# Performance work log

Hardware: AMD Instinct MI355X
Metric: run time of the kernel (lower is better)

## Reference

```python
import jax, jax.numpy as jnp
import numpy as np

D_MODEL = 1024
NUM_HEADS = 16
H_DIM = 4096
EPS = 1e-5


def setup_inputs() -> dict:
    key = jax.random.key(0)
    ks = jax.random.split(key, 16)
    B, S, D, H = 2, 2048, D_MODEL, H_DIM
    s = 0.02
    return {
        "x": jax.random.normal(ks[0], (B, S, D), jnp.float32),
        "wq": jax.random.normal(ks[1], (D, D), jnp.float32) * s,
        "bq": jnp.zeros((D,), jnp.float32),
        "wk": jax.random.normal(ks[2], (D, D), jnp.float32) * s,
        "bk": jnp.zeros((D,), jnp.float32),
        "wv": jax.random.normal(ks[3], (D, D), jnp.float32) * s,
        "bv": jnp.zeros((D,), jnp.float32),
        "wo": jax.random.normal(ks[4], (D, D), jnp.float32) * s,
        "bo": jnp.zeros((D,), jnp.float32),
        "ln1_g": jnp.ones((D,), jnp.float32),
        "ln1_b": jnp.zeros((D,), jnp.float32),
        "w1": jax.random.normal(ks[5], (H, D), jnp.float32) * s,
        "b1": jnp.zeros((H,), jnp.float32),
        "w2": jax.random.normal(ks[6], (D, H), jnp.float32) * s,
        "b2": jnp.zeros((D,), jnp.float32),
        "ln2_g": jnp.ones((D,), jnp.float32),
        "ln2_b": jnp.zeros((D,), jnp.float32),
    }


def _layer_norm(x, g, b):
    mu = jnp.mean(x, axis=-1, keepdims=True)
    var = jnp.mean(jnp.square(x - mu), axis=-1, keepdims=True)
    return (x - mu) * jax.lax.rsqrt(var + EPS) * g + b


def _mhsa(x, wq, bq, wk, bk, wv, bv, wo, bo):
    B, S, D = x.shape
    Hh, hd = NUM_HEADS, D // NUM_HEADS
    q = (x @ wq.T + bq).reshape(B, S, Hh, hd)
    k = (x @ wk.T + bk).reshape(B, S, Hh, hd)
    v = (x @ wv.T + bv).reshape(B, S, Hh, hd)
    scale = hd ** -0.5
    scores = jnp.einsum('bqhd,bkhd->bhqk', q, k) * scale
    att = jax.nn.softmax(scores, axis=-1)
    out = jnp.einsum('bhqk,bkhd->bqhd', att, v).reshape(B, S, D)
    return out @ wo.T + bo


def reference(x, wq, bq, wk, bk, wv, bv, wo, bo, ln1_g, ln1_b,
              w1, b1, w2, b2, ln2_g, ln2_b):
    # pre-norm variant as written in the torch source:
    # x = norm1(x); x = x + msa(x)  (residual uses NORMALIZED x)
    x = _layer_norm(x, ln1_g, ln1_b)
    x = x + _mhsa(x, wq, bq, wk, bk, wv, bv, wo, bo)
    x = _layer_norm(x, ln2_g, ln2_b)
    h = jax.nn.gelu(x @ w1.T + b1, approximate=False)
    x = x + (h @ w2.T + b2)
    return x
```

## Files before the change

### kernel.cpp

```cpp
#include <hip/hip_runtime.h>
#include <hip/hip_bf16.h>

typedef unsigned short u16;
typedef __attribute__((ext_vector_type(8))) short short8;
typedef __attribute__((ext_vector_type(4))) float f32x4;

#define DM 1024
#define HM 4096
#define NHEADS 16
#define HD 64
#define SQ 2048
#define NBATCH 2
#define NTOK 4096

#define NX  ((size_t)NTOK * DM)

__device__ __forceinline__ u16 f2b(float f) {
    union { float f; unsigned int i; } w; w.f = f;
    unsigned int x = w.i;
    return (u16)((x + 0x7FFFu + ((x >> 16) & 1u)) >> 16);
}
__device__ __forceinline__ u16 f2b_ru(float f) {
    union { float f; unsigned int i; } w; w.f = f;
    return (u16)((w.i + 0x8000u) >> 16);
}

__device__ __forceinline__ void gload_lds16(const void* g, void* l) {
    __builtin_amdgcn_global_load_lds(
        (const __attribute__((address_space(1))) void*)g,
        (__attribute__((address_space(3))) void*)l, 16, 0, 0);
}

__global__ void cvt_all(const float* __restrict__ wq, const float* __restrict__ wk,
                        const float* __restrict__ wv, const float* __restrict__ wo,
                        const float* __restrict__ w1, const float* __restrict__ w2,
                        const float* __restrict__ bq, const float* __restrict__ bk,
                        const float* __restrict__ bv, float* __restrict__ bias_dst,
                        u16* __restrict__ dst) {
    const int NW4 = DM * DM / 4;
    int i = blockIdx.x * 256 + threadIdx.x;
    if (i < 12 * NW4) {
        const float* src; int base; float sc = 1.0f;
        if      (i <     NW4) { src = wq; base = 0;       sc = 0.125f; }
        else if (i < 2 * NW4) { src = wk; base = NW4; }
        else if (i < 3 * NW4) { src = wv; base = 2 * NW4; }
        else if (i < 4 * NW4) { src = wo; base = 3 * NW4; }
        else if (i < 8 * NW4) { src = w1; base = 4 * NW4; }
        else                  { src = w2; base = 8 * NW4; }
        float4 f = ((const float4*)src)[i - base];
        ushort4 o;
        o.x = f2b(f.x * sc); o.y = f2b(f.y * sc);
        o.z = f2b(f.z * sc); o.w = f2b(f.w * sc);
        ((ushort4*)dst)[i] = o;
    } else {
        int j = i - 12 * NW4;
        if (j < 3 * DM) {
            float v = (j < DM) ? bq[j] * 0.125f
                    : (j < 2 * DM) ? bk[j - DM] : bv[j - 2 * DM];
            bias_dst[j] = v;
        }
    }
}

__global__ void ln_kernel(const float* __restrict__ xin, const float* __restrict__ g,
                          const float* __restrict__ b, float* __restrict__ outf,
                          u16* __restrict__ outb) {
    int t = blockIdx.x, tid = threadIdx.x;
    float4 f = ((const float4*)(xin + (size_t)t * DM))[tid];
    float v0 = f.x, v1 = f.y, v2 = f.z, v3 = f.w;
    float s  = v0 + v1 + v2 + v3;
    float ss = v0*v0 + v1*v1 + v2*v2 + v3*v3;
    #pragma unroll
    for (int o = 32; o > 0; o >>= 1) {
        s  += __shfl_down(s,  o, 64);
        ss += __shfl_down(ss, o, 64);
    }
    __shared__ float rs[4], rss[4];
    int w = tid >> 6, lane = tid & 63;
    if (!lane) { rs[w] = s; rss[w] = ss; }
    __syncthreads();
    s  = rs[0] + rs[1] + rs[2] + rs[3];
    ss = rss[0] + rss[1] + rss[2] + rss[3];
    float mean = s * (1.0f / DM);
    float var  = ss * (1.0f / DM) - mean * mean;
    float rstd = rsqrtf(var + 1e-5f);
    float4 gu = ((const float4*)g)[tid];
    float4 bu = ((const float4*)b)[tid];
    float4 o;
    o.x = (v0 - mean) * rstd * gu.x + bu.x;
    o.y = (v1 - mean) * rstd * gu.y + bu.y;
    o.z = (v2 - mean) * rstd * gu.z + bu.z;
    o.w = (v3 - mean) * rstd * gu.w + bu.w;
    ((float4*)(outf + (size_t)t * DM))[tid] = o;
    ushort4 ob; ob.x = f2b(o.x); ob.y = f2b(o.y); ob.z = f2b(o.z); ob.w = f2b(o.w);
    ((ushort4*)(outb + (size_t)t * DM))[tid] = ob;
}

__global__ void vtr_kernel(const u16* __restrict__ qkv, u16* __restrict__ vT) {
    __shared__ u16 tile[64][72];
    int bid = blockIdx.x;
    int tt = bid & 31, bh = bid >> 5;
    int h = bh & (NHEADS - 1), b = bh >> 4;
    int tid = threadIdx.x;
    int r = tid >> 2, c0 = (tid & 3) << 4;
    const u16* src = qkv + ((size_t)(b * SQ + tt * 64 + r)) * (3 * DM) + 2 * DM + h * HD + c0;
    #pragma unroll
    for (int j = 0; j < 4; j++)
        *(ushort4*)&tile[r][c0 + (j << 2)] = *(const ushort4*)(src + (j << 2));
    __syncthreads();
    int dd = tid >> 2, t0 = (tid & 3) << 4;
    u16* dst = vT + ((size_t)bh * HD + dd) * SQ + tt * 64 + t0;
    #pragma unroll
    for (int j = 0; j < 4; j++) {
        ushort4 v;
        v.x = tile[t0 + (j << 2) + 0][dd];
        v.y = tile[t0 + (j << 2) + 1][dd];
        v.z = tile[t0 + (j << 2) + 2][dd];
        v.w = tile[t0 + (j << 2) + 3][dd];
        *(ushort4*)(dst + (j << 2)) = v;
    }
}

template<int GELU, int RESID, int OUTBF>
__global__ __launch_bounds__(256, 3)
void gemm_bt(const u16* __restrict__ A, const u16* __restrict__ W,
             const float* __restrict__ bias, const float* __restrict__ resid,
             void* __restrict__ Cout, int M, int N, int K) {
    __shared__ __attribute__((aligned(16))) u16 As[128 * 64];
    __shared__ __attribute__((aligned(16))) u16 Bs[128 * 64];
    int tid  = threadIdx.x;
    int wid  = tid >> 6, lane = tid & 63;
    int m0 = blockIdx.y << 7, n0 = blockIdx.x << 7;
    int wm = (wid & 1) << 6, wn = (wid >> 1) << 6;

    int rIn = lane >> 3;
    int cIn = (lane & 7) << 3;
    int s0  = wid << 2;
    int fr = lane & 15;
    int fc = (lane >> 4) << 3;

    f32x4 acc[4][4];
    #pragma unroll
    for (int i = 0; i < 4; i++)
        #pragma unroll
        for (int j = 0; j < 4; j++)
            acc[i][j] = (f32x4){0.f, 0.f, 0.f, 0.f};

    for (int k0 = 0; k0 < K; k0 += 64) {
        #pragma unroll
        for (int t = 0; t < 4; t++) {
            int s = s0 + t;
            gload_lds16(A + (size_t)(m0 + (s << 3) + rIn) * K + k0 + cIn, As + (s << 9));
            gload_lds16(W + (size_t)(n0 + (s << 3) + rIn) * K + k0 + cIn, Bs + (s << 9));
        }
        __syncthreads();
        #pragma unroll
        for (int ch = 0; ch < 2; ch++) {
            int kc = (ch << 5) + fc;
            short8 af[4], bf[4];
            #pragma unroll
            for (int mi = 0; mi < 4; mi++)
                af[mi] = *(const short8*)(As + (size_t)(wm + (mi << 4) + fr) * 64 + kc);
            #pragma unroll
            for (int ni = 0; ni < 4; ni++)
                bf[ni] = *(const short8*)(Bs + (size_t)(wn + (ni << 4) + fr) * 64 + kc);
            #pragma unroll
            for (int mi = 0; mi < 4; mi++)
                #pragma unroll
                for (int ni = 0; ni < 4; ni++)
                    acc[mi][ni] = __builtin_amdgcn_mfma_f32_16x16x32_bf16(
                        af[mi], bf[ni], acc[mi][ni], 0, 0, 0);
        }
        __syncthreads();
    }

    int erow = (lane >> 4) << 2;
    #pragma unroll
    for (int ni = 0; ni < 4; ni++) {
        int col = n0 + wn + (ni << 4) + fr;
        float bv = bias[col];
        #pragma unroll
        for (int mi = 0; mi < 4; mi++) {
            #pragma unroll
            for (int r = 0; r < 4; r++) {
                int row = m0 + wm + (mi << 4) + erow + r;
                float val = acc[mi][ni][r] + bv;
                if (GELU)  val = 0.5f * val * (1.0f + erff(val * 0.70710678118654752f));
                if (RESID) val += resid[(size_t)row * N + col];
                if (OUTBF) ((u16*)Cout)[(size_t)row * N + col] = f2b(val);
                else       ((float*)Cout)[(size_t)row * N + col] = val;
            }
        }
    }
}

template<int GELU, int RESID, int OUTBF>
__global__ __launch_bounds__(256, 3)
void gemm_n64(const u16* __restrict__ A, const u16* __restrict__ W,
              const float* __restrict__ bias, const float* __restrict__ resid,
              void* __restrict__ Cout, int M, int N, int K) {
    __shared__ __attribute__((aligned(16))) u16 As[128 * 64];
    __shared__ __attribute__((aligned(16))) u16 Bs[64 * 64];
    int tid  = threadIdx.x;
    int wid  = tid >> 6, lane = tid & 63;
    int m0 = blockIdx.y << 7, n0 = blockIdx.x << 6;
    int wm = (wid & 1) << 6, wn = (wid >> 1) << 5;

    int rIn = lane >> 3;
    int cIn = (lane & 7) << 3;
    int sA = wid << 2;
    int sB = wid << 1;
    int fr = lane & 15;
    int fc = (lane >> 4) << 3;

    f32x4 acc[4][2];
    #pragma unroll
    for (int i = 0; i < 4; i++)
        #pragma unroll
        for (int j = 0; j < 2; j++)
            acc[i][j] = (f32x4){0.f, 0.f, 0.f, 0.f};

    for (int k0 = 0; k0 < K; k0 += 64) {
        #pragma unroll
        for (int t = 0; t < 4; t++) {
            int s = sA + t;
            gload_lds16(A + (size_t)(m0 + (s << 3) + rIn) * K + k0 + cIn, As + (s << 9));
        }
        #pragma unroll
        for (int t = 0; t < 2; t++) {
            int s = sB + t;
            gload_lds16(W + (size_t)(n0 + (s << 3) + rIn) * K + k0 + cIn, Bs + (s << 9));
        }
        __syncthreads();
        #pragma unroll
        for (int ch = 0; ch < 2; ch++) {
            int kc = (ch << 5) + fc;
            short8 af[4], bf[2];
            #pragma unroll
            for (int mi = 0; mi < 4; mi++)
                af[mi] = *(const short8*)(As + (size_t)(wm + (mi << 4) + fr) * 64 + kc);
            #pragma unroll
            for (int ni = 0; ni < 2; ni++)
                bf[ni] = *(const short8*)(Bs + (size_t)(wn + (ni << 4) + fr) * 64 + kc);
            #pragma unroll
            for (int mi = 0; mi < 4; mi++)
                #pragma unroll
                for (int ni = 0; ni < 2; ni++)
                    acc[mi][ni] = __builtin_amdgcn_mfma_f32_16x16x32_bf16(
                        af[mi], bf[ni], acc[mi][ni], 0, 0, 0);
        }
        __syncthreads();
    }

    int erow = (lane >> 4) << 2;
    #pragma unroll
    for (int ni = 0; ni < 2; ni++) {
        int col = n0 + wn + (ni << 4) + fr;
        float bv = bias[col];
        #pragma unroll
        for (int mi = 0; mi < 4; mi++) {
            #pragma unroll
            for (int r = 0; r < 4; r++) {
                int row = m0 + wm + (mi << 4) + erow + r;
                float val = acc[mi][ni][r] + bv;
                if (GELU)  val = 0.5f * val * (1.0f + erff(val * 0.70710678118654752f));
                if (RESID) val += resid[(size_t)row * N + col];
                if (OUTBF) ((u16*)Cout)[(size_t)row * N + col] = f2b(val);
                else       ((float*)Cout)[(size_t)row * N + col] = val;
            }
        }
    }
}

__global__ __launch_bounds__(256) void fattn_mfma(const u16* __restrict__ QKV,
                                                  const u16* __restrict__ VT,
                                                  u16* __restrict__ O) {
    __shared__ __attribute__((aligned(16))) u16 QP[4096];
    __shared__ __attribute__((aligned(16))) u16 Ks[2][4096];
    __shared__ __attribute__((aligned(16))) u16 Vt[2][4096];
    const int ld = 3 * DM;
    int bid = blockIdx.x;
    int qt = bid & 31, bh = bid >> 5;
    int h = bh & (NHEADS - 1), b = bh >> 4;
    int tid = threadIdx.x, wid = tid >> 6, lane = tid & 63;
    int fr = lane & 15;
    int fcs = (((lane >> 4) ^ ((fr >> 1) & 3)) << 3);
    int lsw = (((lane & 3) ^ ((lane >> 3) & 3)) << 3);
    size_t tokb = (size_t)b * SQ;
    const u16* Qg  = QKV + tokb * ld + h * HD;
    const u16* Kg  = QKV + tokb * ld + DM + h * HD;
    const u16* VTg = VT + ((size_t)bh * HD) * SQ;
    int s0 = wid << 1;
    u16* Ps = QP + (wid << 10);

    {
        #pragma unroll
        for (int t = 0; t < 2; t++) {
            int s = s0 + t;
            const u16* g = Qg + (size_t)(qt * 64 + ((s & 3) << 4) + (lane >> 2)) * ld
                         + ((s >> 2) << 5) + lsw;
            gload_lds16(g, QP + (s << 9));
        }
    }
    {
        #pragma unroll
        for (int t = 0; t < 2; t++) {
            int s = s0 + t;
            const u16* g = Kg + (size_t)(((s & 3) << 4) + (lane >> 2)) * ld
                         + ((s >> 2) << 5) + lsw;
            gload_lds16(g, Ks[0] + (s << 9));
            const u16* gv = VTg + (size_t)(((s & 3) << 4) + (lane >> 2)) * SQ
                          + ((s >> 2) << 5) + lsw;
            gload_lds16(gv, Vt[0] + (s << 9));
        }
    }
    f32x4 oacc[4];
    #pragma unroll
    for (int di = 0; di < 4; di++) oacc[di] = (f32x4){0.f, 0.f, 0.f, 0.f};
    float lsum[4] = {0.f, 0.f, 0.f, 0.f};
    __syncthreads();
    short8 aq0 = *(const short8*)(QP + ((wid << 4) + fr) * 32 + fcs);
    short8 aq1 = *(const short8*)(QP + 2048 + ((wid << 4) + fr) * 32 + fcs);
    __syncthreads();

    for (int kt = 0; kt < SQ / 64; kt++) {
        int buf = kt & 1;
        if (kt + 1 < SQ / 64) {
            #pragma unroll
            for (int t = 0; t < 2; t++) {
                int s = s0 + t;
                const u16* g = Kg + (size_t)((kt + 1) * 64 + ((s & 3) << 4) + (lane >> 2)) * ld
                             + ((s >> 2) << 5) + lsw;
                gload_lds16(g, Ks[buf ^ 1] + (s << 9));
                const u16* gv = VTg + (size_t)(((s & 3) << 4) + (lane >> 2)) * SQ
                              + (kt + 1) * 64 + ((s >> 2) << 5) + lsw;
                gload_lds16(gv, Vt[buf ^ 1] + (s << 9));
            }
        }
        #pragma unroll
        for (int ni = 0; ni < 4; ni++) {
            short8 bk0 = *(const short8*)(Ks[buf] + ((ni << 4) + fr) * 32 + fcs);
            short8 bk1 = *(const short8*)(Ks[buf] + 2048 + ((ni << 4) + fr) * 32 + fcs);
            f32x4 z = (f32x4){0.f, 0.f, 0.f, 0.f};
            __builtin_amdgcn_s_setprio(1);
            z = __builtin_amdgcn_mfma_f32_16x16x32_bf16(aq0, bk0, z, 0, 0, 0);
            z = __builtin_amdgcn_mfma_f32_16x16x32_bf16(aq1, bk1, z, 0, 0, 0);
            __builtin_amdgcn_s_setprio(0);
            int c  = (ni << 4) + fr;
            int cb = (c >> 5) << 9;
            int khi = (c & 31) >> 3, klo = c & 7;
            #pragma unroll
            for (int r = 0; r < 4; r++) {
                float e = __expf(z[r]);
                lsum[r] += e;
                int row = ((lane >> 4) << 2) + r;
                Ps[cb + row * 32 + ((khi ^ ((row >> 1) & 3)) << 3) + klo] = f2b_ru(e);
            }
        }
        short8 ap0 = *(const short8*)(Ps + fr * 32 + fcs);
        short8 ap1 = *(const short8*)(Ps + 512 + fr * 32 + fcs);
        __builtin_amdgcn_s_setprio(1);
        #pragma unroll
        for (int di = 0; di < 4; di++) {
            short8 bv0 = *(const short8*)(Vt[buf] + ((di << 4) + fr) * 32 + fcs);
            short8 bv1 = *(const short8*)(Vt[buf] + 2048 + ((di << 4) + fr) * 32 + fcs);
            oacc[di] = __builtin_amdgcn_mfma_f32_16x16x32_bf16(ap0, bv0, oacc[di], 0, 0, 0);
            oacc[di] = __builtin_amdgcn_mfma_f32_16x16x32_bf16(ap1, bv1, oacc[di], 0, 0, 0);
        }
        __builtin_amdgcn_s_setprio(0);
        __syncthreads();
    }
    #pragma unroll
    for (int msk = 1; msk <= 8; msk <<= 1)
        #pragma unroll
        for (int r = 0; r < 4; r++) lsum[r] += __shfl_xor(lsum[r], msk, 64);
    float inv[4];
    #pragma unroll
    for (int r = 0; r < 4; r++) inv[r] = 1.0f / lsum[r];
    #pragma unroll
    for (int di = 0; di < 4; di++) {
        int d = (di << 4) + fr;
        #pragma unroll
        for (int r = 0; r < 4; r++) {
            int q = qt * 64 + (wid << 4) + ((lane >> 4) << 2) + r;
            O[(tokb + q) * DM + h * HD + d] = f2b(oacc[di][r] * inv[r]);
        }
    }
}

extern "C" void kernel_launch(void* const* d_in, const int* in_sizes, int n_in,
                              void* d_out, int out_size, void* d_ws, size_t ws_size,
                              hipStream_t stream) {
    if (n_in < 17) return;
    const float* x   = (const float*)d_in[0];
    const float* wq  = (const float*)d_in[1];
    const float* bq  = (const float*)d_in[2];
    const float* wk  = (const float*)d_in[3];
    const float* bk  = (const float*)d_in[4];
    const float* wv  = (const float*)d_in[5];
    const float* bv  = (const float*)d_in[6];
    const float* wo  = (const float*)d_in[7];
    const float* bo  = (const float*)d_in[8];
    const float* g1  = (const float*)d_in[9];
    const float* e1  = (const float*)d_in[10];
    const float* w1  = (const float*)d_in[11];
    const float* b1  = (const float*)d_in[12];
    const float* w2  = (const float*)d_in[13];
    const float* b2  = (const float*)d_in[14];
    const float* g2  = (const float*)d_in[15];
    const float* e2  = (const float*)d_in[16];

    float* F = (float*)d_ws;
    size_t off = 0;
    float* xnf   = F + off; off += NX;
    u16*   xnb   = (u16*)(F + off); off += NX / 2;
    u16*   qkvb  = (u16*)(F + off); off += (size_t)NTOK * 3 * DM / 2;
    u16*   vTb   = (u16*)(F + off); off += (size_t)NTOK * DM / 2;
    float* y     = F + off; off += NX;
    u16*   aob   = (u16*)(F + off); off += NX / 2;
    u16*   hb    = (u16*)(F + off); off += (size_t)NTOK * HM / 2;
    u16*   wqkvb = (u16*)(F + off); off += (size_t)3 * DM * DM / 2;
    u16*   wob   = (u16*)(F + off); off += (size_t)DM * DM / 2;
    u16*   w1b   = (u16*)(F + off); off += (size_t)HM * DM / 2;
    u16*   w2b   = (u16*)(F + off); off += (size_t)DM * HM / 2;
    float* bqkv  = F + off; off += 3 * DM;
    if (ws_size < off * sizeof(float)) return;

    dim3 blk(256);
    cvt_all<<<(12 * DM * DM / 4 + 3 * DM + 255) / 256, blk, 0, stream>>>(
        wq, wk, wv, wo, w1, w2, bq, bk, bv, bqkv, wqkvb);

    ln_kernel<<<NTOK, blk, 0, stream>>>(x, g1, e1, xnf, xnb);
    gemm_bt<0,0,1><<<dim3(3 * DM / 128, NTOK / 128), blk, 0, stream>>>(
        xnb, wqkvb, bqkv, nullptr, qkvb, NTOK, 3 * DM, DM);
    vtr_kernel<<<NBATCH * NHEADS * (SQ / 64), blk, 0, stream>>>(qkvb, vTb);
    fattn_mfma<<<NBATCH * NHEADS * (SQ / 64), blk, 0, stream>>>(qkvb, vTb, aob);
    gemm_n64<0,1,0><<<dim3(DM / 64, NTOK / 128), blk, 0, stream>>>(
        aob, wob, bo, xnf, y, NTOK, DM, DM);
    ln_kernel<<<NTOK, blk, 0, stream>>>(y, g2, e2, xnf, xnb);
    gemm_bt<1,0,1><<<dim3(HM / 128, NTOK / 128), blk, 0, stream>>>(
        xnb, w1b, b1, nullptr, hb, NTOK, HM, DM);
    gemm_n64<0,1,0><<<dim3(DM / 64, NTOK / 128), blk, 0, stream>>>(
        hb, w2b, b2, xnf, d_out, NTOK, DM, HM);
}
```

Before: 405.6 us.

## Double-buffer GEMM LDS tiles and XOR-swizzle columns to avoid bank conflicts

Both GEMM kernels now keep two LDS buffers and prefetch the next K tile while computing the current one, so global loads can overlap MFMA work. The K-column chunks are XOR-swizzled by row on load and read, to reduce LDS bank conflicts on the fragment reads. LDS use per block doubles and the occupancy hint drops from 3 to 2 blocks per CU, which may reduce latency hiding from concurrent blocks.

```diff
diff --git a/kernel.cpp b/kernel.cpp
--- a/kernel.cpp
+++ b/kernel.cpp
@@ -122,22 +122,23 @@
 }
 
 template<int GELU, int RESID, int OUTBF>
-__global__ __launch_bounds__(256, 3)
+__global__ __launch_bounds__(256, 2)
 void gemm_bt(const u16* __restrict__ A, const u16* __restrict__ W,
              const float* __restrict__ bias, const float* __restrict__ resid,
              void* __restrict__ Cout, int M, int N, int K) {
-    __shared__ __attribute__((aligned(16))) u16 As[128 * 64];
-    __shared__ __attribute__((aligned(16))) u16 Bs[128 * 64];
+    __shared__ __attribute__((aligned(16))) u16 As[2 * 128 * 64];
+    __shared__ __attribute__((aligned(16))) u16 Bs[2 * 128 * 64];
     int tid  = threadIdx.x;
     int wid  = tid >> 6, lane = tid & 63;
     int m0 = blockIdx.y << 7, n0 = blockIdx.x << 7;
     int wm = (wid & 1) << 6, wn = (wid >> 1) << 6;
 
     int rIn = lane >> 3;
-    int cIn = (lane & 7) << 3;
+    int cSw = (((lane & 7) ^ (lane >> 3)) << 3);
     int s0  = wid << 2;
     int fr = lane & 15;
-    int fc = (lane >> 4) << 3;
+    int ksw0 = (((lane >> 4) ^ (lane & 7)) << 3);
+    int ksw1 = (((4 + (lane >> 4)) ^ (lane & 7)) << 3);
 
     f32x4 acc[4][4];
     #pragma unroll
@@ -146,24 +147,39 @@
         for (int j = 0; j < 4; j++)
             acc[i][j] = (f32x4){0.f, 0.f, 0.f, 0.f};
 
-    for (int k0 = 0; k0 < K; k0 += 64) {
-        #pragma unroll
-        for (int t = 0; t < 4; t++) {
-            int s = s0 + t;
-            gload_lds16(A + (size_t)(m0 + (s << 3) + rIn) * K + k0 + cIn, As + (s << 9));
-            gload_lds16(W + (size_t)(n0 + (s << 3) + rIn) * K + k0 + cIn, Bs + (s << 9));
-        }
-        __syncthreads();
+    #pragma unroll
+    for (int t = 0; t < 4; t++) {
+        int s = s0 + t;
+        gload_lds16(A + (size_t)(m0 + (s << 3) + rIn) * K + cSw, As + (s << 9));
+        gload_lds16(W + (size_t)(n0 + (s << 3) + rIn) * K + cSw, Bs + (s << 9));
+    }
+    __syncthreads();
+
+    int nk = K >> 6;
+    for (int kt = 0; kt < nk; kt++) {
+        int buf = kt & 1;
+        const u16* Ab = As + (buf << 13);
+        const u16* Bb = Bs + (buf << 13);
+        if (kt + 1 < nk) {
+            int k0 = (kt + 1) << 6;
+            int bo = (buf ^ 1) << 13;
+            #pragma unroll
+            for (int t = 0; t < 4; t++) {
+                int s = s0 + t;
+                gload_lds16(A + (size_t)(m0 + (s << 3) + rIn) * K + k0 + cSw, As + bo + (s << 9));
+                gload_lds16(W + (size_t)(n0 + (s << 3) + rIn) * K + k0 + cSw, Bs + bo + (s << 9));
+            }
+        }
         #pragma unroll
         for (int ch = 0; ch < 2; ch++) {
-            int kc = (ch << 5) + fc;
+            int ks = ch ? ksw1 : ksw0;
             short8 af[4], bf[4];
             #pragma unroll
             for (int mi = 0; mi < 4; mi++)
-                af[mi] = *(const short8*)(As + (size_t)(wm + (mi << 4) + fr) * 64 + kc);
+                af[mi] = *(const short8*)(Ab + (size_t)(wm + (mi << 4) + fr) * 64 + ks);
             #pragma unroll
             for (int ni = 0; ni < 4; ni++)
-                bf[ni] = *(const short8*)(Bs + (size_t)(wn + (ni << 4) + fr) * 64 + kc);
+                bf[ni] = *(const short8*)(Bb + (size_t)(wn + (ni << 4) + fr) * 64 + ks);
             #pragma unroll
             for (int mi = 0; mi < 4; mi++)
                 #pragma unroll
@@ -199,19 +215,20 @@
 void gemm_n64(const u16* __restrict__ A, const u16* __restrict__ W,
               const float* __restrict__ bias, const float* __restrict__ resid,
               void* __restrict__ Cout, int M, int N, int K) {
-    __shared__ __attribute__((aligned(16))) u16 As[128 * 64];
-    __shared__ __attribute__((aligned(16))) u16 Bs[64 * 64];
+    __shared__ __attribute__((aligned(16))) u16 As[2 * 128 * 64];
+    __shared__ __attribute__((aligned(16))) u16 Bs[2 * 64 * 64];
     int tid  = threadIdx.x;
     int wid  = tid >> 6, lane = tid & 63;
     int m0 = blockIdx.y << 7, n0 = blockIdx.x << 6;
     int wm = (wid & 1) << 6, wn = (wid >> 1) << 5;
 
     int rIn = lane >> 3;
-    int cIn = (lane & 7) << 3;
+    int cSw = (((lane & 7) ^ (lane >> 3)) << 3);
     int sA = wid << 2;
     int sB = wid << 1;
     int fr = lane & 15;
-    int fc = (lane >> 4) << 3;
+    int ksw0 = (((lane >> 4) ^ (lane & 7)) << 3);
+    int ksw1 = (((4 + (lane >> 4)) ^ (lane & 7)) << 3);
 
     f32x4 acc[4][2];
     #pragma unroll
@@ -220,28 +237,48 @@
         for (int j = 0; j < 2; j++)
             acc[i][j] = (f32x4){0.f, 0.f, 0.f, 0.f};
 
-    for (int k0 = 0; k0 < K; k0 += 64) {
-        #pragma unroll
-        for (int t = 0; t < 4; t++) {
-            int s = sA + t;
-            gload_lds16(A + (size_t)(m0 + (s << 3) + rIn) * K + k0 + cIn, As + (s << 9));
-        }
-        #pragma unroll
-        for (int t = 0; t < 2; t++) {
-            int s = sB + t;
-            gload_lds16(W + (size_t)(n0 + (s << 3) + rIn) * K + k0 + cIn, Bs + (s << 9));
-        }
-        __syncthreads();
+    #pragma unroll
+    for (int t = 0; t < 4; t++) {
+        int s = sA + t;
+        gload_lds16(A + (size_t)(m0 + (s << 3) + rIn) * K + cSw, As + (s << 9));
+    }
+    #pragma unroll
+    for (int t = 0; t < 2; t++) {
+        int s = sB + t;
+        gload_lds16(W + (size_t)(n0 + (s << 3) + rIn) * K + cSw, Bs + (s << 9));
+    }
+    __syncthreads();
+
+    int nk = K >> 6;
+    for (int kt = 0; kt < nk; kt++) {
+        int buf = kt & 1;
+        const u16* Ab = As + (buf << 13);
+        const u16* Bb = Bs + (buf << 12);
+        if (kt + 1 < nk) {
+            int k0 = (kt + 1) << 6;
+            int boA = (buf ^ 1) << 13;
+            int boB = (buf ^ 1) << 12;
+            #pragma unroll
+            for (int t = 0; t < 4; t++) {
+                int s = sA + t;
+                gload_lds16(A + (size_t)(m0 + (s << 3) + rIn) * K + k0 + cSw, As + boA + (s << 9));
+            }
+            #pragma unroll
+            for (int t = 0; t < 2; t++) {
+                int s = sB + t;
+                gload_lds16(W + (size_t)(n0 + (s << 3) + rIn) * K + k0 + cSw, Bs + boB + (s << 9));
+            }
+        }
         #pragma unroll
         for (int ch = 0; ch < 2; ch++) {
-            int kc = (ch << 5) + fc;
+            int ks = ch ? ksw1 : ksw0;
             short8 af[4], bf[2];
             #pragma unroll
             for (int mi = 0; mi < 4; mi++)
-                af[mi] = *(const short8*)(As + (size_t)(wm + (mi << 4) + fr) * 64 + kc);
+                af[mi] = *(const short8*)(Ab + (size_t)(wm + (mi << 4) + fr) * 64 + ks);
             #pragma unroll
             for (int ni = 0; ni < 2; ni++)
-                bf[ni] = *(const short8*)(Bs + (size_t)(wn + (ni << 4) + fr) * 64 + kc);
+                bf[ni] = *(const short8*)(Bb + (size_t)(wn + (ni << 4) + fr) * 64 + ks);
             #pragma unroll
             for (int mi = 0; mi < 4; mi++)
                 #pragma unroll
```

Measured after the change: 386.9 us. 1.05x faster.
